# Optimization experiments

Measured on AMD Instinct MI355X. Metric: run time of the kernel, lower is better.

## Reference

```python
import jax, jax.numpy as jnp
import numpy as np

B, T, D_MODEL, N_HEADS = 4, 2048, 1024, 16
HEAD_DIM = D_MODEL // N_HEADS


def setup_inputs() -> dict:
    key = jax.random.key(0)
    ks = jax.random.split(key, 5)
    s = 0.02  # small init scale for weights
    return {
        "x": jax.random.normal(ks[0], (B, T, D_MODEL), dtype=jnp.float32),
        "Wq": jax.random.normal(ks[1], (D_MODEL, D_MODEL), dtype=jnp.float32) * s,
        "Wk": jax.random.normal(ks[2], (D_MODEL, D_MODEL), dtype=jnp.float32) * s,
        "Wv": jax.random.normal(ks[3], (D_MODEL, D_MODEL), dtype=jnp.float32) * s,
        "Wo": jax.random.normal(ks[4], (D_MODEL, D_MODEL), dtype=jnp.float32) * s,
        "bo": jnp.zeros((D_MODEL,), dtype=jnp.float32),
    }


def reference(x, Wq, Wk, Wv, Wo, bo):
    b, t, c = x.shape
    h, d = N_HEADS, HEAD_DIM
    # QKV projections (no bias), split into heads: [B, T, H, D]
    Q = (x @ Wq).reshape(b, t, h, d)
    K = (x @ Wk).reshape(b, t, h, d)
    V = (x @ Wv).reshape(b, t, h, d)
    # attention scores [B, H, T, T]
    scores = jnp.einsum("bqhd,bkhd->bhqk", Q, K)
    causal = jnp.tril(jnp.ones((t, t), dtype=bool))  # True = keep
    scores = jnp.where(causal, scores, -jnp.inf)
    weights = jax.nn.softmax(scores / jnp.sqrt(jnp.float32(d)), axis=-1)
    # dropout with p=0.0 is identity
    ctx = jnp.einsum("bhqk,bkhd->bqhd", weights, V).reshape(b, t, c)
    return ctx @ Wo + bo
```

## Files before the change

kernel.cpp:

```cpp
#include <hip/hip_runtime.h>
#include <math.h>

#define TB 2048
#define NB 4
#define NH 16
#define HD 64
#define DM 1024
#define MROWS (NB * TB)
#define QBLK 128

typedef unsigned short u16;
typedef __attribute__((ext_vector_type(8))) _Float16 f16x8;
typedef __attribute__((ext_vector_type(2))) __fp16 fp16x2;
typedef __attribute__((ext_vector_type(8))) u16 u16x8;
typedef __attribute__((ext_vector_type(4))) u16 u16x4;
typedef __attribute__((ext_vector_type(4))) float f32x4;

#define SZE ((size_t)MROWS * DM)
#define WSZE ((size_t)DM * DM)

#define QSCALE 0.1803368801111204f
#define DEFER_THR 8.0f

#define PHI(r) ((((r) & 3) << 1) | (((r) >> 3) & 1))

__device__ __forceinline__ u16 f2h(float f) {
    _Float16 h = (_Float16)f;
    union { _Float16 h; u16 u; } c; c.h = h;
    return c.u;
}

__device__ __forceinline__ void gload16(const u16* g, u16* l) {
    __builtin_amdgcn_global_load_lds(
        (const __attribute__((address_space(1))) void*)g,
        (__attribute__((address_space(3))) void*)l, 16, 0, 0);
}

#define MFMA16(a, b, c) __builtin_amdgcn_mfma_f32_16x16x32_f16((a), (b), (c), 0, 0, 0)

__global__ __launch_bounds__(256) void convert_x(const float* __restrict__ x,
                                                 u16* __restrict__ xh)
{
    size_t i = ((size_t)blockIdx.x * 256 + threadIdx.x) * 8;
    float4 a = *(const float4*)(x + i);
    float4 b = *(const float4*)(x + i + 4);
    float v[8] = {a.x, a.y, a.z, a.w, b.x, b.y, b.z, b.w};
    u16x8 hi;
#pragma unroll
    for (int j = 0; j < 8; ++j) hi[j] = f2h(v[j]);
    *(u16x8*)(xh + i) = hi;
}

__global__ __launch_bounds__(256) void convert_wt(const float* __restrict__ Wq,
                                                  const float* __restrict__ Wk,
                                                  const float* __restrict__ Wv,
                                                  const float* __restrict__ Wo,
                                                  u16* __restrict__ wt)
{
    const int z = blockIdx.z;
    const float* W = (z == 0) ? Wq : (z == 1) ? Wk : (z == 2) ? Wv : Wo;
    u16* dh = wt + (size_t)z * WSZE;
    __shared__ float tile[64][65];
    const int tid = threadIdx.x;
    const int k0 = blockIdx.x * 64, n0 = blockIdx.y * 64;
#pragma unroll
    for (int i = 0; i < 4; ++i) {
        int c = i * 256 + tid, r = c >> 4, c4 = (c & 15) << 2;
        *(float4*)&tile[r][c4] = *(const float4*)&W[(size_t)(k0 + r) * DM + n0 + c4];
    }
    __syncthreads();
#pragma unroll
    for (int i = 0; i < 4; ++i) {
        int c = i * 256 + tid, n = c >> 4, k4 = (c & 15) << 2;
        u16x4 hi;
#pragma unroll
        for (int j = 0; j < 4; ++j) hi[j] = f2h(tile[k4 + j][n]);
        *(u16x4*)(dh + (size_t)(n0 + n) * DM + k0 + k4) = hi;
    }
}

__device__ __forceinline__ void gemm_nt_128(const u16* __restrict__ A,
                                            const u16* __restrict__ B,
                                            int bm, int bn, u16* lds,
                                            f32x4 acc[4][4])
{
    const int tid = threadIdx.x, lane = tid & 63;
    const int wid = tid >> 6, wm = wid >> 1, wn = wid & 1;
    const int lr = lane & 15, g = lane >> 4;
    u16* sA = lds;
    u16* sB = lds + 4096;

#pragma unroll
    for (int i = 0; i < 4; ++i)
#pragma unroll
        for (int j = 0; j < 4; ++j) acc[i][j] = (f32x4)0.f;

    for (int k0 = 0; k0 < DM; k0 += 32) {
        __syncthreads();
#pragma unroll
        for (int i = 0; i < 2; ++i) {
            int c = i * 256 + tid, r = c >> 2, db = c & 3;
            int src = db ^ ((r >> 1) & 3);
            size_t ga = (size_t)(bm + r) * DM + k0 + src * 8;
            size_t gb = (size_t)(bn + r) * DM + k0 + src * 8;
            gload16(A + ga, sA + c * 8);
            gload16(B + gb, sB + c * 8);
        }
        __syncthreads();

        f16x8 ah[4], bhv[4];
#pragma unroll
        for (int f = 0; f < 4; ++f) {
            int ra = wm * 64 + f * 16 + lr;
            int oa = ra * 32 + ((g ^ ((ra >> 1) & 3)) << 3);
            ah[f] = *(const f16x8*)(sA + oa);
            int rb = wn * 64 + f * 16 + lr;
            int ob = rb * 32 + ((g ^ ((rb >> 1) & 3)) << 3);
            bhv[f] = *(const f16x8*)(sB + ob);
        }
#pragma unroll
        for (int fi = 0; fi < 4; ++fi)
#pragma unroll
            for (int fj = 0; fj < 4; ++fj)
                acc[fi][fj] = MFMA16(ah[fi], bhv[fj], acc[fi][fj]);
    }
}

__global__ __launch_bounds__(256) void qkv_gemm(const u16* __restrict__ xh,
                                                const u16* __restrict__ wt,
                                                u16* __restrict__ qkvb)
{
    __shared__ u16 lds[8192];
    const int z = blockIdx.z;
    const u16* Bw = wt + (size_t)z * WSZE;
    const int bm = blockIdx.x * 128, bn = blockIdx.y * 128;

    f32x4 acc[4][4];
    gemm_nt_128(xh, Bw, bm, bn, lds, acc);

    const int lane = threadIdx.x & 63, wid = threadIdx.x >> 6;
    const int wm = wid >> 1, wn = wid & 1;
    const int lr = lane & 15, g = lane >> 4;

    if (z < 2) {
        const float scale = (z == 0) ? QSCALE : 1.0f;
        u16* outh = qkvb + (size_t)z * SZE;
#pragma unroll
        for (int fi = 0; fi < 4; ++fi)
#pragma unroll
            for (int fj = 0; fj < 4; ++fj)
#pragma unroll
                for (int reg = 0; reg < 4; ++reg) {
                    int m = bm + wm * 64 + fi * 16 + g * 4 + reg;
                    int n = bn + wn * 64 + fj * 16 + lr;
                    int b = m >> 11, t = m & (TB - 1);
                    int h = n >> 6, d = n & 63;
                    size_t o = ((size_t)(b * NH + h) * TB + t) * HD + d;
                    outh[o] = f2h(acc[fi][fj][reg] * scale);
                }
    } else {
        u16* vth = qkvb + (size_t)2 * SZE;
#pragma unroll
        for (int fi = 0; fi < 4; ++fi)
#pragma unroll
            for (int fj = 0; fj < 4; ++fj) {
                int n = bn + wn * 64 + fj * 16 + lr;
                int h = n >> 6, d = n & 63;
                int m0 = bm + wm * 64 + fi * 16 + g * 4;
                int b = m0 >> 11, t = m0 & (TB - 1);
                u16x4 v4;
#pragma unroll
                for (int reg = 0; reg < 4; ++reg) v4[reg] = f2h(acc[fi][fj][reg]);
                *(u16x4*)(vth + ((size_t)(b * NH + h) * HD + d) * TB + t) = v4;
            }
    }
}

__global__ __launch_bounds__(256) void proj_gemm(const u16* __restrict__ ch,
                                                 const u16* __restrict__ Bw,
                                                 const float* __restrict__ bo,
                                                 float* __restrict__ out)
{
    __shared__ u16 lds[8192];
    const int bm = blockIdx.x * 128, bn = blockIdx.y * 128;
    f32x4 acc[4][4];
    gemm_nt_128(ch, Bw, bm, bn, lds, acc);

    const int lane = threadIdx.x & 63, wid = threadIdx.x >> 6;
    const int wm = wid >> 1, wn = wid & 1;
    const int lr = lane & 15, g = lane >> 4;
#pragma unroll
    for (int fi = 0; fi < 4; ++fi)
#pragma unroll
        for (int fj = 0; fj < 4; ++fj) {
            int n = bn + wn * 64 + fj * 16 + lr;
            float bias = bo[n];
#pragma unroll
            for (int reg = 0; reg < 4; ++reg) {
                int m = bm + wm * 64 + fi * 16 + g * 4 + reg;
                out[(size_t)m * DM + n] = acc[fi][fj][reg] + bias;
            }
        }
}

__device__ __forceinline__ void stage_tile(const u16* __restrict__ Kh,
                                           const u16* __restrict__ Vth,
                                           size_t bh, int k0, u16* dst, int tid)
{
    int r = tid >> 3, sl = tid & 7;
    int src = sl ^ PHI(r);
    size_t gk = (bh * TB + k0 + r) * HD + src * 8;
    gload16(Kh + gk, dst + tid * 8);
    size_t gv = (bh * HD + r) * TB + k0 + src * 8;
    gload16(Vth + gv, dst + 4096 + tid * 8);
}

__global__ __launch_bounds__(512, 4) void attn_kernel(const u16* __restrict__ Qh,
                                                      const u16* __restrict__ Kh,
                                                      const u16* __restrict__ Vth,
                                                      u16* __restrict__ ctxh)
{
    __shared__ u16 lds[16384];

    const int tid = threadIdx.x, lane = tid & 63, wid = tid >> 6;
    const int lr = lane & 15, g = lane >> 4;

    const int f = blockIdx.x;
    const int xcd = f & 7, slot = f >> 3;
    const int bh_idx = xcd * 8 + (slot >> 4);
    const int qi = 15 - (slot & 15);
    const int b = bh_idx >> 4, h = bh_idx & 15;

    const int q0 = qi * QBLK;
    const size_t bh = (size_t)(b * NH + h);
    const int nt = 2 * qi + 2;
    const int wq0 = q0 + wid * 16;
    const int qrow = wq0 + lr;

    f16x8 qa[2];
    {
        size_t rowoff = (bh * TB + qrow) * HD;
#pragma unroll
        for (int ks = 0; ks < 2; ++ks)
            qa[ks] = *(const f16x8*)(Qh + rowoff + ks * 32 + g * 8);
    }

    f32x4 o[4];
#pragma unroll
    for (int i = 0; i < 4; ++i) o[i] = (f32x4)0.f;
    float mrun = -INFINITY, lrun = 0.f;

    stage_tile(Kh, Vth, bh, 0, lds, tid);

    for (int kt = 0; kt < nt; ++kt) {
        __syncthreads();
        if (kt + 1 < nt)
            stage_tile(Kh, Vth, bh, (kt + 1) * 64, lds + ((kt + 1) & 1) * 8192, tid);

        const int k0 = kt * 64;
        if (k0 > wq0 + 15) continue;

        u16* sK = lds + (kt & 1) * 8192;
        u16* sV = sK + 4096;

        f32x4 s[4];
#pragma unroll
        for (int fj = 0; fj < 4; ++fj) {
            s[fj] = (f32x4)0.f;
            int R = 32 * (fj >> 1) + 8 * (lr >> 2) + 4 * (fj & 1) + (lr & 3);
#pragma unroll
            for (int ks = 0; ks < 2; ++ks) {
                int sl = (ks * 4 + g) ^ PHI(R);
                f16x8 kb = *(const f16x8*)(sK + R * 64 + sl * 8);
                s[fj] = MFMA16(kb, qa[ks], s[fj]);
            }
        }

        if ((k0 + 63) > wq0) {
#pragma unroll
            for (int fj = 0; fj < 4; ++fj)
#pragma unroll
                for (int reg = 0; reg < 4; ++reg) {
                    int key = k0 + 32 * (fj >> 1) + 8 * g + 4 * (fj & 1) + reg;
                    if (key > qrow) s[fj][reg] = -INFINITY;
                }
        }

        float mloc = -INFINITY;
#pragma unroll
        for (int fj = 0; fj < 4; ++fj)
#pragma unroll
            for (int reg = 0; reg < 4; ++reg) mloc = fmaxf(mloc, s[fj][reg]);
        mloc = fmaxf(mloc, __shfl_xor(mloc, 16));
        mloc = fmaxf(mloc, __shfl_xor(mloc, 32));

        if (mloc > mrun + DEFER_THR) {
            float scx = exp2f(mrun - mloc);
            lrun *= scx;
#pragma unroll
            for (int fd = 0; fd < 4; ++fd) o[fd] *= scx;
            mrun = mloc;
        }

        float p[4][4];
        float rs = 0.f;
#pragma unroll
        for (int fj = 0; fj < 4; ++fj)
#pragma unroll
            for (int reg = 0; reg < 4; ++reg) {
                p[fj][reg] = exp2f(s[fj][reg] - mrun);
                rs += p[fj][reg];
            }
        rs += __shfl_xor(rs, 16);
        rs += __shfl_xor(rs, 32);
        lrun += rs;

        union { f16x8 v8; fp16x2 v2[4]; } pb0, pb1;
        pb0.v2[0] = __builtin_amdgcn_cvt_pkrtz(p[0][0], p[0][1]);
        pb0.v2[1] = __builtin_amdgcn_cvt_pkrtz(p[0][2], p[0][3]);
        pb0.v2[2] = __builtin_amdgcn_cvt_pkrtz(p[1][0], p[1][1]);
        pb0.v2[3] = __builtin_amdgcn_cvt_pkrtz(p[1][2], p[1][3]);
        pb1.v2[0] = __builtin_amdgcn_cvt_pkrtz(p[2][0], p[2][1]);
        pb1.v2[1] = __builtin_amdgcn_cvt_pkrtz(p[2][2], p[2][3]);
        pb1.v2[2] = __builtin_amdgcn_cvt_pkrtz(p[3][0], p[3][1]);
        pb1.v2[3] = __builtin_amdgcn_cvt_pkrtz(p[3][2], p[3][3]);

#pragma unroll
        for (int fd = 0; fd < 4; ++fd) {
            int Rv = fd * 16 + lr;
#pragma unroll
            for (int ks = 0; ks < 2; ++ks) {
                int sl = (ks * 4 + g) ^ PHI(Rv);
                f16x8 vb = *(const f16x8*)(sV + Rv * 64 + sl * 8);
                o[fd] = MFMA16(vb, ks ? pb1.v8 : pb0.v8, o[fd]);
            }
        }
    }

    float inv = 1.f / lrun;
#pragma unroll
    for (int fd = 0; fd < 4; ++fd) {
        u16x4 st;
#pragma unroll
        for (int reg = 0; reg < 4; ++reg) st[reg] = f2h(o[fd][reg] * inv);
        int d = fd * 16 + 4 * g;
        *(u16x4*)(ctxh + ((size_t)b * TB + qrow) * DM + h * HD + d) = st;
    }
}

extern "C" void kernel_launch(void* const* d_in, const int* in_sizes, int n_in,
                              void* d_out, int out_size, void* d_ws, size_t ws_size,
                              hipStream_t stream)
{
    const float* x  = (const float*)d_in[0];
    const float* Wq = (const float*)d_in[1];
    const float* Wk = (const float*)d_in[2];
    const float* Wv = (const float*)d_in[3];
    const float* Wo = (const float*)d_in[4];
    const float* bo = (const float*)d_in[5];
    float* out = (float*)d_out;

    u16* w = (u16*)d_ws;
    u16* xh   = w;
    u16* wt   = w + SZE;
    u16* qkvb = w + SZE + 4 * WSZE;
    u16* qh   = qkvb;
    u16* kh   = qkvb + SZE;
    u16* vth  = qkvb + 2 * SZE;
    u16* ctxh = xh;

    convert_x<<<dim3(4096), 256, 0, stream>>>(x, xh);
    convert_wt<<<dim3(16, 16, 4), 256, 0, stream>>>(Wq, Wk, Wv, Wo, wt);
    qkv_gemm<<<dim3(MROWS / 128, DM / 128, 3), 256, 0, stream>>>(xh, wt, qkvb);
    attn_kernel<<<dim3(TB / QBLK * NH * NB), 512, 0, stream>>>(qh, kh, vth, ctxh);
    proj_gemm<<<dim3(MROWS / 128, DM / 128), 256, 0, stream>>>(
        ctxh, wt + 3 * WSZE, bo, out);
}
```

Before: 284.8 us.

## Pair causal query blocks per attention CTA, XCD-aware GEMM remap, MFMA priority

The attention kernel now gives each block two query tiles (qi = 8+pp and 7-pp), so every block does a balanced amount of causal work, and the grid halves to 512 blocks. The QKV and projection GEMMs switch to a flat 1D grid, with tiles remapped so each XCD gets a contiguous band of M rows, aiming at better L2 reuse. s_setprio is placed around the MFMA sections to favour the matrix-core issuing waves. The tradeoff is fewer attention blocks, which may leave the 256 CUs with less parallelism and less latency hiding, plus an extra sync between the two halves.

```diff
diff --git a/kernel.cpp b/kernel.cpp
--- a/kernel.cpp
+++ b/kernel.cpp
@@ -118,11 +118,13 @@
             int ob = rb * 32 + ((g ^ ((rb >> 1) & 3)) << 3);
             bhv[f] = *(const f16x8*)(sB + ob);
         }
+        __builtin_amdgcn_s_setprio(1);
 #pragma unroll
         for (int fi = 0; fi < 4; ++fi)
 #pragma unroll
             for (int fj = 0; fj < 4; ++fj)
                 acc[fi][fj] = MFMA16(ah[fi], bhv[fj], acc[fi][fj]);
+        __builtin_amdgcn_s_setprio(0);
     }
 }
 
@@ -131,9 +133,16 @@
                                                 u16* __restrict__ qkvb)
 {
     __shared__ u16 lds[8192];
-    const int z = blockIdx.z;
+    const int f = blockIdx.x;
+    const int xcd = f & 7, s = f >> 3;
+    const int ntz = s >> 3;
+    const int z = ntz >> 3;
+    const int nt = ntz & 7;
+    const int mt = s & 7;
+    const int bm = (xcd * 8 + mt) * 128;
+    const int bn = nt * 128;
+
     const u16* Bw = wt + (size_t)z * WSZE;
-    const int bm = blockIdx.x * 128, bn = blockIdx.y * 128;
 
     f32x4 acc[4][4];
     gemm_nt_128(xh, Bw, bm, bn, lds, acc);
@@ -182,7 +191,12 @@
                                                  float* __restrict__ out)
 {
     __shared__ u16 lds[8192];
-    const int bm = blockIdx.x * 128, bn = blockIdx.y * 128;
+    const int f = blockIdx.x;
+    const int xcd = f & 7, s = f >> 3;
+    const int nt = s >> 3, mt = s & 7;
+    const int bm = (xcd * 8 + mt) * 128;
+    const int bn = nt * 128;
+
     f32x4 acc[4][4];
     gemm_nt_128(ch, Bw, bm, bn, lds, acc);
 
@@ -226,125 +240,134 @@
     const int lr = lane & 15, g = lane >> 4;
 
     const int f = blockIdx.x;
-    const int xcd = f & 7, slot = f >> 3;
-    const int bh_idx = xcd * 8 + (slot >> 4);
-    const int qi = 15 - (slot & 15);
+    const int xcd = f & 7, s = f >> 3;
+    const int bh_idx = xcd * 8 + (s >> 3);
+    const int pp = s & 7;
     const int b = bh_idx >> 4, h = bh_idx & 15;
-
-    const int q0 = qi * QBLK;
     const size_t bh = (size_t)(b * NH + h);
-    const int nt = 2 * qi + 2;
-    const int wq0 = q0 + wid * 16;
-    const int qrow = wq0 + lr;
-
-    f16x8 qa[2];
-    {
-        size_t rowoff = (bh * TB + qrow) * HD;
-#pragma unroll
-        for (int ks = 0; ks < 2; ++ks)
-            qa[ks] = *(const f16x8*)(Qh + rowoff + ks * 32 + g * 8);
-    }
-
-    f32x4 o[4];
-#pragma unroll
-    for (int i = 0; i < 4; ++i) o[i] = (f32x4)0.f;
-    float mrun = -INFINITY, lrun = 0.f;
-
-    stage_tile(Kh, Vth, bh, 0, lds, tid);
-
-    for (int kt = 0; kt < nt; ++kt) {
-        __syncthreads();
-        if (kt + 1 < nt)
-            stage_tile(Kh, Vth, bh, (kt + 1) * 64, lds + ((kt + 1) & 1) * 8192, tid);
-
-        const int k0 = kt * 64;
-        if (k0 > wq0 + 15) continue;
-
-        u16* sK = lds + (kt & 1) * 8192;
-        u16* sV = sK + 4096;
-
-        f32x4 s[4];
-#pragma unroll
-        for (int fj = 0; fj < 4; ++fj) {
-            s[fj] = (f32x4)0.f;
-            int R = 32 * (fj >> 1) + 8 * (lr >> 2) + 4 * (fj & 1) + (lr & 3);
-#pragma unroll
-            for (int ks = 0; ks < 2; ++ks) {
-                int sl = (ks * 4 + g) ^ PHI(R);
-                f16x8 kb = *(const f16x8*)(sK + R * 64 + sl * 8);
-                s[fj] = MFMA16(kb, qa[ks], s[fj]);
-            }
-        }
-
-        if ((k0 + 63) > wq0) {
+
+    for (int half = 0; half < 2; ++half) {
+        const int qi = half ? (7 - pp) : (8 + pp);
+        const int q0 = qi * QBLK;
+        const int nt = 2 * qi + 2;
+        const int wq0 = q0 + wid * 16;
+        const int qrow = wq0 + lr;
+
+        f16x8 qa[2];
+        {
+            size_t rowoff = (bh * TB + qrow) * HD;
+#pragma unroll
+            for (int ks = 0; ks < 2; ++ks)
+                qa[ks] = *(const f16x8*)(Qh + rowoff + ks * 32 + g * 8);
+        }
+
+        f32x4 o[4];
+#pragma unroll
+        for (int i = 0; i < 4; ++i) o[i] = (f32x4)0.f;
+        float mrun = -INFINITY, lrun = 0.f;
+
+        if (half) __syncthreads();
+        stage_tile(Kh, Vth, bh, 0, lds, tid);
+
+        for (int kt = 0; kt < nt; ++kt) {
+            __syncthreads();
+            if (kt + 1 < nt)
+                stage_tile(Kh, Vth, bh, (kt + 1) * 64,
+                           lds + ((kt + 1) & 1) * 8192, tid);
+
+            const int k0 = kt * 64;
+            if (k0 > wq0 + 15) continue;
+
+            u16* sK = lds + (kt & 1) * 8192;
+            u16* sV = sK + 4096;
+
+            f32x4 sv[4];
+            __builtin_amdgcn_s_setprio(1);
+#pragma unroll
+            for (int fj = 0; fj < 4; ++fj) {
+                sv[fj] = (f32x4)0.f;
+                int R = 32 * (fj >> 1) + 8 * (lr >> 2) + 4 * (fj & 1) + (lr & 3);
+#pragma unroll
+                for (int ks = 0; ks < 2; ++ks) {
+                    int sl = (ks * 4 + g) ^ PHI(R);
+                    f16x8 kb = *(const f16x8*)(sK + R * 64 + sl * 8);
+                    sv[fj] = MFMA16(kb, qa[ks], sv[fj]);
+                }
+            }
+            __builtin_amdgcn_s_setprio(0);
+
+            if ((k0 + 63) > wq0) {
+#pragma unroll
+                for (int fj = 0; fj < 4; ++fj)
+#pragma unroll
+                    for (int reg = 0; reg < 4; ++reg) {
+                        int key = k0 + 32 * (fj >> 1) + 8 * g + 4 * (fj & 1) + reg;
+                        if (key > qrow) sv[fj][reg] = -INFINITY;
+                    }
+            }
+
+            float mloc = -INFINITY;
 #pragma unroll
             for (int fj = 0; fj < 4; ++fj)
 #pragma unroll
+                for (int reg = 0; reg < 4; ++reg) mloc = fmaxf(mloc, sv[fj][reg]);
+            mloc = fmaxf(mloc, __shfl_xor(mloc, 16));
+            mloc = fmaxf(mloc, __shfl_xor(mloc, 32));
+
+            if (mloc > mrun + DEFER_THR) {
+                float scx = exp2f(mrun - mloc);
+                lrun *= scx;
+#pragma unroll
+                for (int fd = 0; fd < 4; ++fd) o[fd] *= scx;
+                mrun = mloc;
+            }
+
+            float p[4][4];
+            float rs = 0.f;
+#pragma unroll
+            for (int fj = 0; fj < 4; ++fj)
+#pragma unroll
                 for (int reg = 0; reg < 4; ++reg) {
-                    int key = k0 + 32 * (fj >> 1) + 8 * g + 4 * (fj & 1) + reg;
-                    if (key > qrow) s[fj][reg] = -INFINITY;
+                    p[fj][reg] = exp2f(sv[fj][reg] - mrun);
+                    rs += p[fj][reg];
                 }
-        }
-
-        float mloc = -INFINITY;
-#pragma unroll
-        for (int fj = 0; fj < 4; ++fj)
-#pragma unroll
-            for (int reg = 0; reg < 4; ++reg) mloc = fmaxf(mloc, s[fj][reg]);
-        mloc = fmaxf(mloc, __shfl_xor(mloc, 16));
-        mloc = fmaxf(mloc, __shfl_xor(mloc, 32));
-
-        if (mloc > mrun + DEFER_THR) {
-            float scx = exp2f(mrun - mloc);
-            lrun *= scx;
-#pragma unroll
-            for (int fd = 0; fd < 4; ++fd) o[fd] *= scx;
-            mrun = mloc;
-        }
-
-        float p[4][4];
-        float rs = 0.f;
-#pragma unroll
-        for (int fj = 0; fj < 4; ++fj)
-#pragma unroll
-            for (int reg = 0; reg < 4; ++reg) {
-                p[fj][reg] = exp2f(s[fj][reg] - mrun);
-                rs += p[fj][reg];
-            }
-        rs += __shfl_xor(rs, 16);
-        rs += __shfl_xor(rs, 32);
-        lrun += rs;
-
-        union { f16x8 v8; fp16x2 v2[4]; } pb0, pb1;
-        pb0.v2[0] = __builtin_amdgcn_cvt_pkrtz(p[0][0], p[0][1]);
-        pb0.v2[1] = __builtin_amdgcn_cvt_pkrtz(p[0][2], p[0][3]);
-        pb0.v2[2] = __builtin_amdgcn_cvt_pkrtz(p[1][0], p[1][1]);
-        pb0.v2[3] = __builtin_amdgcn_cvt_pkrtz(p[1][2], p[1][3]);
-        pb1.v2[0] = __builtin_amdgcn_cvt_pkrtz(p[2][0], p[2][1]);
-        pb1.v2[1] = __builtin_amdgcn_cvt_pkrtz(p[2][2], p[2][3]);
-        pb1.v2[2] = __builtin_amdgcn_cvt_pkrtz(p[3][0], p[3][1]);
-        pb1.v2[3] = __builtin_amdgcn_cvt_pkrtz(p[3][2], p[3][3]);
-
+            rs += __shfl_xor(rs, 16);
+            rs += __shfl_xor(rs, 32);
+            lrun += rs;
+
+            union { f16x8 v8; fp16x2 v2[4]; } pb0, pb1;
+            pb0.v2[0] = __builtin_amdgcn_cvt_pkrtz(p[0][0], p[0][1]);
+            pb0.v2[1] = __builtin_amdgcn_cvt_pkrtz(p[0][2], p[0][3]);
+            pb0.v2[2] = __builtin_amdgcn_cvt_pkrtz(p[1][0], p[1][1]);
+            pb0.v2[3] = __builtin_amdgcn_cvt_pkrtz(p[1][2], p[1][3]);
+            pb1.v2[0] = __builtin_amdgcn_cvt_pkrtz(p[2][0], p[2][1]);
+            pb1.v2[1] = __builtin_amdgcn_cvt_pkrtz(p[2][2], p[2][3]);
+            pb1.v2[2] = __builtin_amdgcn_cvt_pkrtz(p[3][0], p[3][1]);
+            pb1.v2[3] = __builtin_amdgcn_cvt_pkrtz(p[3][2], p[3][3]);
+
+            __builtin_amdgcn_s_setprio(1);
+#pragma unroll
+            for (int fd = 0; fd < 4; ++fd) {
+                int Rv = fd * 16 + lr;
+#pragma unroll
+                for (int ks = 0; ks < 2; ++ks) {
+                    int sl = (ks * 4 + g) ^ PHI(Rv);
+                    f16x8 vb = *(const f16x8*)(sV + Rv * 64 + sl * 8);
+                    o[fd] = MFMA16(vb, ks ? pb1.v8 : pb0.v8, o[fd]);
+                }
+            }
+            __builtin_amdgcn_s_setprio(0);
+        }
+
+        float inv = 1.f / lrun;
 #pragma unroll
         for (int fd = 0; fd < 4; ++fd) {
-            int Rv = fd * 16 + lr;
-#pragma unroll
-            for (int ks = 0; ks < 2; ++ks) {
-                int sl = (ks * 4 + g) ^ PHI(Rv);
-                f16x8 vb = *(const f16x8*)(sV + Rv * 64 + sl * 8);
-                o[fd] = MFMA16(vb, ks ? pb1.v8 : pb0.v8, o[fd]);
-            }
-        }
-    }
-
-    float inv = 1.f / lrun;
-#pragma unroll
-    for (int fd = 0; fd < 4; ++fd) {
-        u16x4 st;
-#pragma unroll
-        for (int reg = 0; reg < 4; ++reg) st[reg] = f2h(o[fd][reg] * inv);
-        int d = fd * 16 + 4 * g;
-        *(u16x4*)(ctxh + ((size_t)b * TB + qrow) * DM + h * HD + d) = st;
+            u16x4 st;
+#pragma unroll
+            for (int reg = 0; reg < 4; ++reg) st[reg] = f2h(o[fd][reg] * inv);
+            int d = fd * 16 + 4 * g;
+            *(u16x4*)(ctxh + ((size_t)b * TB + qrow) * DM + h * HD + d) = st;
+        }
     }
 }
 
@@ -371,8 +394,7 @@
 
     convert_x<<<dim3(4096), 256, 0, stream>>>(x, xh);
     convert_wt<<<dim3(16, 16, 4), 256, 0, stream>>>(Wq, Wk, Wv, Wo, wt);
-    qkv_gemm<<<dim3(MROWS / 128, DM / 128, 3), 256, 0, stream>>>(xh, wt, qkvb);
-    attn_kernel<<<dim3(TB / QBLK * NH * NB), 512, 0, stream>>>(qh, kh, vth, ctxh);
-    proj_gemm<<<dim3(MROWS / 128, DM / 128), 256, 0, stream>>>(
-        ctxh, wt + 3 * WSZE, bo, out);
-}
+    qkv_gemm<<<dim3(1536), 256, 0, stream>>>(xh, wt, qkvb);
+    attn_kernel<<<dim3(512), 512, 0, stream>>>(qh, kh, vth, ctxh);
+    proj_gemm<<<dim3(512), 256, 0, stream>>>(ctxh, wt + 3 * WSZE, bo, out);
+}
```

Result: faster. 264.8 us (-7.0%).
